# Kernel optimization log

Measured on AMD Instinct MI355X. Metric: run time of the kernel, lower is better.

The kernel has to match this reference:

```python
import jax, jax.numpy as jnp
import numpy as np

V, C, TCTX, H, L = 32000, 768, 1024, 12, 6
B, T = 2, 1024
D = C // H
EPS = 1e-5


def setup_inputs() -> dict:
    key = jax.random.key(0)
    ks = jax.random.split(key, 12)
    s = lambda k, shape: jax.random.normal(k, shape, jnp.float32) * 0.02
    return {
        "x_indices": jax.random.randint(ks[0], (B, T), 0, V, jnp.int32),
        "tok_emb": s(ks[1], (V, C)),
        "pos_emb": s(ks[2], (TCTX, C)),
        "ln1_g": jnp.ones((L, C)), "ln1_b": jnp.zeros((L, C)),
        "wq": s(ks[3], (L, C, C)), "wk": s(ks[4], (L, C, C)), "wv": s(ks[5], (L, C, C)),
        "wo": s(ks[6], (L, C, C)), "bo": jnp.zeros((L, C)),
        "ln2_g": jnp.ones((L, C)), "ln2_b": jnp.zeros((L, C)),
        "w1": s(ks[7], (L, C, 4 * C)), "b1": jnp.zeros((L, 4 * C)),
        "w2": s(ks[8], (L, 4 * C, C)), "b2": jnp.zeros((L, C)),
        "lnf_g": jnp.ones((C,)), "lnf_b": jnp.zeros((C,)),
        "wp": s(ks[9], (C, V)), "bp": jnp.zeros((V,)),
    }


def _ln(x, g, b):
    m = x.mean(-1, keepdims=True)
    v = ((x - m) ** 2).mean(-1, keepdims=True)
    return (x - m) * jax.lax.rsqrt(v + EPS) * g + b


def _forward(x_indices, tok_emb, pos_emb, ln1_g, ln1_b, wq, wk, wv, wo, bo,
             ln2_g, ln2_b, w1, b1, w2, b2, lnf_g, lnf_b, wp, bp):
    Bv, Tv = x_indices.shape
    x = tok_emb[x_indices] + pos_emb[:Tv]  # [B,T,C]
    mask = jnp.tril(jnp.ones((Tv, Tv), dtype=bool))  # causal

    def block(x, p):
        g1, be1, q_w, k_w, v_w, o_w, o_b, g2, be2, f1, fb1, f2, fb2 = p
        h = _ln(x, g1, be1)
        q = (h @ q_w).reshape(Bv, Tv, H, D)
        k = (h @ k_w).reshape(Bv, Tv, H, D)
        v = (h @ v_w).reshape(Bv, Tv, H, D)
        scores = jnp.einsum('bthd,bshd->bhts', q, k) / jnp.sqrt(jnp.float32(D))
        scores = jnp.where(mask, scores, -jnp.inf)
        a = jax.nn.softmax(scores, axis=-1)
        o = jnp.einsum('bhts,bshd->bthd', a, v).reshape(Bv, Tv, C)
        x = x + o @ o_w + o_b
        h2 = _ln(x, g2, be2)
        x = x + jax.nn.relu(h2 @ f1 + fb1) @ f2 + fb2
        return x, None

    layer_params = (ln1_g, ln1_b, wq, wk, wv, wo, bo, ln2_g, ln2_b, w1, b1, w2, b2)
    x, _ = jax.lax.scan(block, x, layer_params)
    x = _ln(x, lnf_g, lnf_b)
    return x @ wp + bp  # logits [B,T,V]


def reference(x_indices, tok_emb, pos_emb, ln1_g, ln1_b, wq, wk, wv, wo, bo,
              ln2_g, ln2_b, w1, b1, w2, b2, lnf_g, lnf_b, wp, bp):
    return _forward(x_indices, tok_emb, pos_emb, ln1_g, ln1_b, wq, wk, wv, wo, bo,
                    ln2_g, ln2_b, w1, b1, w2, b2, lnf_g, lnf_b, wp, bp)
```

## Files before the change

### kernel.cpp

```cpp
#include <hip/hip_runtime.h>
#include <stdint.h>

#define DEV __device__ __forceinline__

typedef unsigned short u16;
typedef __attribute__((ext_vector_type(8))) short short8;
typedef __attribute__((ext_vector_type(4))) float floatx4;

#define B_ 2
#define T_ 1024
#define C_ 768
#define H_ 12
#define L_ 6
#define V_ 32000
#define F_ 3072
#define M_ 2048
#define C3_ 2304

#define VMW(n) asm volatile("s_waitcnt vmcnt(" #n ")" ::: "memory")

DEV u16 f2bf(float f) {
  unsigned int u; __builtin_memcpy(&u, &f, 4);
  u += 0x7FFFu + ((u >> 16) & 1u);
  return (u16)(u >> 16);
}

DEV void gload16(const void* g, void* l) {
  __builtin_amdgcn_global_load_lds(
      (__attribute__((address_space(1))) void*)(uintptr_t)g,
      (__attribute__((address_space(3))) void*)(unsigned int)(uintptr_t)l,
      16, 0, 0);
}

DEV int xcd_swz(int flat, int nwg) {
  int q = nwg >> 3, r = nwg & 7;
  int xcd = flat & 7, sid = flat >> 3;
  return (xcd < r ? xcd * (q + 1) : r * (q + 1) + (xcd - r) * q) + sid;
}

__global__ __launch_bounds__(256) void transpose_f32_bf16(
    const float* __restrict__ src, u16* __restrict__ dst, int R, int Cc,
    size_t src_z, size_t dst_z) {
  __shared__ float tile[32][33];
  const float* s = src + (size_t)blockIdx.z * src_z;
  u16* d = dst + (size_t)blockIdx.z * dst_z;
  int c0 = blockIdx.x * 32, r0 = blockIdx.y * 32;
  int tx = threadIdx.x & 31, ty = threadIdx.x >> 5;
#pragma unroll
  for (int i = 0; i < 4; i++)
    tile[ty + 8 * i][tx] = s[(size_t)(r0 + ty + 8 * i) * Cc + (c0 + tx)];
  __syncthreads();
#pragma unroll
  for (int i = 0; i < 4; i++)
    d[(size_t)(c0 + ty + 8 * i) * R + (r0 + tx)] = f2bf(tile[tx][ty + 8 * i]);
}

__global__ __launch_bounds__(256) void embed_kernel(
    const int* __restrict__ idx, const float* __restrict__ tok,
    const float* __restrict__ pos, float* __restrict__ x) {
  int row = blockIdx.x;
  int t = row & (T_ - 1);
  int tk = idx[row];
  const float* tp = tok + (size_t)tk * C_;
  const float* pp = pos + (size_t)t * C_;
  float* xp = x + (size_t)row * C_;
  for (int c = threadIdx.x; c < C_; c += 256) xp[c] = tp[c] + pp[c];
}

__global__ __launch_bounds__(256) void ln_kernel(
    const float* __restrict__ x, const float* __restrict__ g,
    const float* __restrict__ b, u16* __restrict__ out) {
  int row = blockIdx.x;
  int tid = threadIdx.x;
  const float* xp = x + (size_t)row * C_;
  float v0 = xp[tid], v1 = xp[tid + 256], v2 = xp[tid + 512];
  float s = v0 + v1 + v2;
  float ss = v0 * v0 + v1 * v1 + v2 * v2;
#pragma unroll
  for (int o = 32; o > 0; o >>= 1) { s += __shfl_down(s, o); ss += __shfl_down(ss, o); }
  __shared__ float red[8];
  int wid = tid >> 6;
  if ((tid & 63) == 0) { red[wid] = s; red[4 + wid] = ss; }
  __syncthreads();
  float tot = red[0] + red[1] + red[2] + red[3];
  float tss = red[4] + red[5] + red[6] + red[7];
  float mean = tot * (1.f / C_);
  float var = tss * (1.f / C_) - mean * mean;
  float rstd = rsqrtf(var + 1e-5f);
  u16* op = out + (size_t)row * C_;
  op[tid]       = f2bf((v0 - mean) * rstd * g[tid]       + b[tid]);
  op[tid + 256] = f2bf((v1 - mean) * rstd * g[tid + 256] + b[tid + 256]);
  op[tid + 512] = f2bf((v2 - mean) * rstd * g[tid + 512] + b[tid + 512]);
}

template <int THREADS, int BM, int BN, int WM, int WN, int BIAS, int RELU, int OUTMODE, int SPLITK>
__global__ __launch_bounds__(THREADS) void gemm3(
    const u16* __restrict__ A, const u16* __restrict__ BT,
    const float* __restrict__ bias,
    u16* __restrict__ ob, float* __restrict__ fout, u16* __restrict__ vt,
    int N, int K) {
  constexpr int ALOADS = (BM * 64) / (THREADS * 16);
  constexpr int BLOADS = (BN * 64) / (THREADS * 16);
  constexpr int LDS_L = ALOADS + BLOADS;
  constexpr int MF = BM / (WM * 16);
  constexpr int NF = BN / (WN * 16);
  __shared__ __align__(16) u16 As[3][BM * 32];
  __shared__ __align__(16) u16 Bs[3][BN * 32];

  int tid = threadIdx.x;
  int lane = tid & 63, w = tid >> 6;
  int wm = w / WN, wn = w % WN;
  int rr = lane & 15, qg = lane >> 4;

  int gx = gridDim.x;
  int nwg = gx * gridDim.y;
  int flat = blockIdx.y * gx + blockIdx.x;
  int wg = xcd_swz(flat, nwg);
  int m0 = (wg % gx) * BM, n0 = (wg / gx) * BN;

  int kz = SPLITK > 1 ? blockIdx.z : 0;
  int Keff = SPLITK > 1 ? (K / SPLITK) : K;
  int kbase = kz * Keff;

  const u16* Aps[ALOADS];
  const u16* Bps[BLOADS];
#pragma unroll
  for (int i = 0; i < ALOADS; i++) {
    int idx = i * THREADS + tid;
    int row = idx >> 2;
    int chunk = (idx & 3) ^ ((row >> 1) & 3);
    Aps[i] = A + (size_t)(m0 + row) * K + chunk * 8 + kbase;
  }
#pragma unroll
  for (int i = 0; i < BLOADS; i++) {
    int idx = i * THREADS + tid;
    int row = idx >> 2;
    int chunk = (idx & 3) ^ ((row >> 1) & 3);
    Bps[i] = BT + (size_t)(n0 + row) * K + chunk * 8 + kbase;
  }

  auto stage = [&](int sl, int kk) {
#pragma unroll
    for (int i = 0; i < ALOADS; i++)
      gload16(Aps[i] + kk, (char*)As + (size_t)sl * BM * 64 + i * THREADS * 16 + w * 1024);
#pragma unroll
    for (int i = 0; i < BLOADS; i++)
      gload16(Bps[i] + kk, (char*)Bs + (size_t)sl * BN * 64 + i * THREADS * 16 + w * 1024);
  };

  floatx4 zero = {0.f, 0.f, 0.f, 0.f};
  floatx4 acc[MF][NF];
#pragma unroll
  for (int i = 0; i < MF; i++)
#pragma unroll
    for (int j = 0; j < NF; j++) acc[i][j] = zero;

  int NT = Keff >> 5;
  stage(0, 0);
  stage(1, 32);
  if constexpr (LDS_L == 3) VMW(3);
  else if constexpr (LDS_L == 4) VMW(4);
  else VMW(6);
  __builtin_amdgcn_s_barrier();
  __builtin_amdgcn_sched_barrier(0);

  int sqA = (qg ^ ((rr >> 1) & 3)) << 4;

  for (int t = 0; t < NT; ++t) {
    int sl = t % 3;
    if (t + 2 < NT) stage((t + 2) % 3, (t + 2) << 5);
    __builtin_amdgcn_sched_barrier(0);
    const char* Ab = (const char*)As + (size_t)sl * BM * 64;
    const char* Bb = (const char*)Bs + (size_t)sl * BN * 64;
    short8 af[MF], bf[NF];
#pragma unroll
    for (int i = 0; i < MF; i++)
      af[i] = *(const short8*)(Ab + ((wm * (BM / WM) + i * 16 + rr) << 6) + sqA);
#pragma unroll
    for (int j = 0; j < NF; j++)
      bf[j] = *(const short8*)(Bb + ((wn * (BN / WN) + j * 16 + rr) << 6) + sqA);
    __builtin_amdgcn_s_setprio(1);
#pragma unroll
    for (int i = 0; i < MF; i++)
#pragma unroll
      for (int j = 0; j < NF; j++)
        acc[i][j] = __builtin_amdgcn_mfma_f32_16x16x32_bf16(af[i], bf[j], acc[i][j], 0, 0, 0);
    __builtin_amdgcn_s_setprio(0);
    if (t < NT - 2) {
      if constexpr (LDS_L == 3) VMW(3);
      else if constexpr (LDS_L == 4) VMW(4);
      else VMW(6);
    } else if (t == NT - 2) VMW(0);
    if (t < NT - 1) { __builtin_amdgcn_s_barrier(); __builtin_amdgcn_sched_barrier(0); }
  }

  int cb = n0 + wn * (BN / WN);
  int rb = m0 + wm * (BM / WM);
  bool isv = (OUTMODE == 3) && (n0 >= 1536);
#pragma unroll
  for (int i = 0; i < MF; i++) {
#pragma unroll
    for (int j = 0; j < NF; j++) {
      int col = cb + j * 16 + rr;
      float bv = 0.f;
      if (BIAS && kz == 0) bv = bias[col];
      float vals[4];
#pragma unroll
      for (int r = 0; r < 4; r++) {
        float val = acc[i][j][r] + bv;
        if (RELU) val = fmaxf(val, 0.f);
        vals[r] = val;
      }
      int row0 = rb + i * 16 + qg * 4;
      if (isv) {
        int colv = col - 1536;
        int bb = row0 >> 10, t0 = row0 & (T_ - 1);
        uint2 pk;
        pk.x = (unsigned int)f2bf(vals[0]) | ((unsigned int)f2bf(vals[1]) << 16);
        pk.y = (unsigned int)f2bf(vals[2]) | ((unsigned int)f2bf(vals[3]) << 16);
        *(uint2*)&vt[((size_t)bb * C_ + colv) * T_ + t0] = pk;
      } else {
#pragma unroll
        for (int r = 0; r < 4; r++) {
          size_t o = (size_t)(row0 + r) * N + col;
          if (OUTMODE == 0 || OUTMODE == 3) ob[o] = f2bf(vals[r]);
          else if (OUTMODE == 1) {
            if (SPLITK > 1) atomicAdd(&fout[o], vals[r]);
            else fout[o] += vals[r];
          } else fout[o] = vals[r];
        }
      }
    }
  }
}

__global__ __launch_bounds__(512, 2) void gemm8(
    const u16* __restrict__ A, const u16* __restrict__ BT,
    const float* __restrict__ bias, float* __restrict__ fout, int N, int K) {
  __shared__ __align__(16) u16 As[2][2][256 * 32];
  __shared__ __align__(16) u16 Bs[2][2][256 * 32];
  int tid = threadIdx.x;
  int lane = tid & 63, w = tid >> 6;
  int wr = w >> 2, wc = w & 3;
  int rr = lane & 15, qg = lane >> 4;

  int gx = gridDim.x;
  int nwg = gx * gridDim.y;
  int flat = blockIdx.y * gx + blockIdx.x;
  int wg = xcd_swz(flat, nwg);
  int m0 = (wg % gx) * 256, n0 = (wg / gx) * 256;

  int r0 = tid >> 2;
  int c0 = (((tid & 3) ^ ((r0 >> 1) & 3)) << 3);
  int r1 = (512 + tid) >> 2;
  int c1 = (((tid & 3) ^ ((r1 >> 1) & 3)) << 3);
  const u16* Asrc0 = A + (size_t)(m0 + r0) * K + c0;
  const u16* Asrc1 = A + (size_t)(m0 + r1) * K + c1;
  const u16* Bsrc0 = BT + (size_t)(n0 + r0) * K + c0;
  const u16* Bsrc1 = BT + (size_t)(n0 + r1) * K + c1;

  auto stageA = [&](int s, int kh, int kt) {
    int koff = (kt << 6) + (kh << 5);
    gload16(Asrc0 + koff, (char*)&As[s][kh][0] + w * 1024);
    gload16(Asrc1 + koff, (char*)&As[s][kh][0] + 8192 + w * 1024);
  };
  auto stageB = [&](int s, int kh, int kt) {
    int koff = (kt << 6) + (kh << 5);
    gload16(Bsrc0 + koff, (char*)&Bs[s][kh][0] + w * 1024);
    gload16(Bsrc1 + koff, (char*)&Bs[s][kh][0] + 8192 + w * 1024);
  };

  floatx4 zero = {0.f, 0.f, 0.f, 0.f};
  floatx4 acc[8][4];
#pragma unroll
  for (int i = 0; i < 8; i++)
#pragma unroll
    for (int j = 0; j < 4; j++) acc[i][j] = zero;

  int NKT = K >> 6;
  stageA(0, 0, 0); stageB(0, 0, 0); stageA(0, 1, 0); stageB(0, 1, 0);
  VMW(0);
  __builtin_amdgcn_s_barrier();
  __builtin_amdgcn_sched_barrier(0);

  int sq = (qg ^ ((rr >> 1) & 3)) << 4;
  short8 bf[4];

  for (int kt = 0; kt < NKT; ++kt) {
    int d = kt & 1;
    bool more = (kt + 1) < NKT;
#pragma unroll
    for (int p = 0; p < 4; ++p) {
      const int kh = p >> 1, rh = p & 1;
      const char* Ab = (const char*)&As[d][kh][0];
      const char* Bb = (const char*)&Bs[d][kh][0];
      short8 af[4];
#pragma unroll
      for (int i = 0; i < 4; i++)
        af[i] = *(const short8*)(Ab + ((wr * 128 + rh * 64 + i * 16 + rr) << 6) + sq);
      if (rh == 0) {
#pragma unroll
        for (int j = 0; j < 4; j++)
          bf[j] = *(const short8*)(Bb + ((wc * 64 + j * 16 + rr) << 6) + sq);
      }
      if (more) {
        if (p == 0) stageA(d ^ 1, 0, kt + 1);
        else if (p == 1) stageB(d ^ 1, 0, kt + 1);
        else if (p == 2) stageA(d ^ 1, 1, kt + 1);
        else stageB(d ^ 1, 1, kt + 1);
      }
      __builtin_amdgcn_s_barrier();
      asm volatile("s_waitcnt lgkmcnt(0)" ::: "memory");
      __builtin_amdgcn_sched_barrier(0);
      __builtin_amdgcn_s_setprio(1);
#pragma unroll
      for (int i = 0; i < 4; i++)
#pragma unroll
        for (int j = 0; j < 4; j++)
          acc[rh * 4 + i][j] =
              __builtin_amdgcn_mfma_f32_16x16x32_bf16(af[i], bf[j], acc[rh * 4 + i][j], 0, 0, 0);
      __builtin_amdgcn_s_setprio(0);
      if (rh == 1) VMW(4);
      __builtin_amdgcn_s_barrier();
      __builtin_amdgcn_sched_barrier(0);
    }
  }

  int cb = n0 + wc * 64;
  int rb = m0 + wr * 128;
#pragma unroll
  for (int fi = 0; fi < 8; fi++) {
#pragma unroll
    for (int j = 0; j < 4; j++) {
      int col = cb + j * 16 + rr;
      float bv = bias[col];
      int row0 = rb + fi * 16 + qg * 4;
#pragma unroll
      for (int r = 0; r < 4; r++)
        fout[(size_t)(row0 + r) * N + col] = acc[fi][j][r] + bv;
    }
  }
}

__global__ __launch_bounds__(64) void attn_kernel(
    const u16* __restrict__ qkv, const u16* __restrict__ vt, u16* __restrict__ o) {
  __shared__ __align__(16) u16 P_s[16 * 48];
  int nwg = gridDim.x;
  int wg = xcd_swz(blockIdx.x, nwg);
  int qt = wg & 63;
  int h = (wg >> 6) % H_;
  int b = wg / (64 * H_);
  int q0 = qt << 4;
  int lane = threadIdx.x;
  int rr = lane & 15, qg = lane >> 4, kq = qg << 3;

  const u16* qb = qkv + (size_t)(b * T_ + q0 + rr) * C3_ + h * 64;
  short8 qf0 = *(const short8*)(qb + kq);
  short8 qf1 = *(const short8*)(qb + 32 + kq);

  float m_r = -1e30f, l_r = 0.f;
  floatx4 zero = {0.f, 0.f, 0.f, 0.f};
  floatx4 oacc[4];
#pragma unroll
  for (int d = 0; d < 4; d++) oacc[d] = zero;

  const u16* kbase = qkv + (size_t)(b * T_) * C3_ + 768 + h * 64;
  const u16* vbase = vt + (size_t)(b * C_ + h * 64) * T_;

  for (int kt0 = 0; kt0 <= q0 + 15; kt0 += 32) {
    floatx4 s[2];
#pragma unroll
    for (int c = 0; c < 2; c++) {
      const u16* kb = kbase + (size_t)(kt0 + c * 16 + rr) * C3_;
      short8 kf0 = *(const short8*)(kb + kq);
      short8 kf1 = *(const short8*)(kb + 32 + kq);
      floatx4 z = zero;
      z = __builtin_amdgcn_mfma_f32_16x16x32_bf16(kf0, qf0, z, 0, 0, 0);
      z = __builtin_amdgcn_mfma_f32_16x16x32_bf16(kf1, qf1, z, 0, 0, 0);
      s[c] = z;
    }
    int qpos = q0 + rr;
    float p[2][4];
    float mx = -1e30f;
#pragma unroll
    for (int c = 0; c < 2; c++)
#pragma unroll
      for (int r = 0; r < 4; r++) {
        int kpos = kt0 + c * 16 + qg * 4 + r;
        float val = s[c][r] * 0.125f;
        val = (kpos <= qpos) ? val : -1e30f;
        p[c][r] = val;
        mx = fmaxf(mx, val);
      }
    mx = fmaxf(mx, __shfl_xor(mx, 16));
    mx = fmaxf(mx, __shfl_xor(mx, 32));
    float mn = fmaxf(m_r, mx);
    float escL = exp2f((m_r - mn) * 1.44269504f);
    m_r = mn;
    float ps = 0.f;
#pragma unroll
    for (int c = 0; c < 2; c++)
#pragma unroll
      for (int r = 0; r < 4; r++) {
        float pv = exp2f((p[c][r] - mn) * 1.44269504f);
        p[c][r] = pv;
        ps += pv;
      }
    ps += __shfl_xor(ps, 16);
    ps += __shfl_xor(ps, 32);
    l_r = l_r * escL + ps;
#pragma unroll
    for (int c = 0; c < 2; c++) {
      unsigned int u0 = (unsigned int)f2bf(p[c][0]) | ((unsigned int)f2bf(p[c][1]) << 16);
      unsigned int u1 = (unsigned int)f2bf(p[c][2]) | ((unsigned int)f2bf(p[c][3]) << 16);
      uint2 pk; pk.x = u0; pk.y = u1;
      *(uint2*)&P_s[rr * 48 + c * 16 + qg * 4] = pk;
    }
    float er[4];
#pragma unroll
    for (int r = 0; r < 4; r++) er[r] = __shfl(escL, qg * 4 + r);
#pragma unroll
    for (int d = 0; d < 4; d++)
#pragma unroll
      for (int r = 0; r < 4; r++) oacc[d][r] *= er[r];
    short8 pa = *(const short8*)&P_s[rr * 48 + kq];
#pragma unroll
    for (int d = 0; d < 4; d++) {
      short8 vf = *(const short8*)(vbase + (size_t)(d * 16 + rr) * T_ + kt0 + kq);
      oacc[d] = __builtin_amdgcn_mfma_f32_16x16x32_bf16(pa, vf, oacc[d], 0, 0, 0);
    }
  }
  float lb[4];
#pragma unroll
  for (int r = 0; r < 4; r++) lb[r] = __shfl(l_r, qg * 4 + r);
  u16* obp = o + (size_t)(b * T_ + q0) * C_ + h * 64;
#pragma unroll
  for (int d = 0; d < 4; d++)
#pragma unroll
    for (int r = 0; r < 4; r++) {
      int row = qg * 4 + r;
      obp[(size_t)row * C_ + d * 16 + rr] = f2bf(oacc[d][r] / lb[r]);
    }
}

extern "C" void kernel_launch(void* const* d_in, const int* in_sizes, int n_in,
                              void* d_out, int out_size, void* d_ws, size_t ws_size,
                              hipStream_t stream) {
  (void)in_sizes; (void)n_in; (void)out_size; (void)ws_size;
  const int*   xidx = (const int*)d_in[0];
  const float* tok  = (const float*)d_in[1];
  const float* pos  = (const float*)d_in[2];
  const float* ln1g = (const float*)d_in[3];
  const float* ln1b = (const float*)d_in[4];
  const float* wq   = (const float*)d_in[5];
  const float* wk   = (const float*)d_in[6];
  const float* wv   = (const float*)d_in[7];
  const float* wo   = (const float*)d_in[8];
  const float* bo   = (const float*)d_in[9];
  const float* ln2g = (const float*)d_in[10];
  const float* ln2b = (const float*)d_in[11];
  const float* w1   = (const float*)d_in[12];
  const float* b1   = (const float*)d_in[13];
  const float* w2   = (const float*)d_in[14];
  const float* b2   = (const float*)d_in[15];
  const float* lnfg = (const float*)d_in[16];
  const float* lnfb = (const float*)d_in[17];
  const float* wp   = (const float*)d_in[18];
  const float* bp   = (const float*)d_in[19];

  char* ws = (char*)d_ws;
  size_t off = 0;
  auto alloc = [&](size_t bytes) { char* p = ws + off; off += (bytes + 255) & ~(size_t)255; return p; };
  u16* wqkvT = (u16*)alloc((size_t)L_ * 3 * C_ * C_ * 2);
  u16* woT = (u16*)alloc((size_t)L_ * C_ * C_ * 2);
  u16* w1T = (u16*)alloc((size_t)L_ * C_ * F_ * 2);
  u16* w2T = (u16*)alloc((size_t)L_ * C_ * F_ * 2);
  u16* wpT = (u16*)alloc((size_t)C_ * V_ * 2);
  float* x = (float*)alloc((size_t)M_ * C_ * 4);
  u16* hb   = (u16*)alloc((size_t)M_ * C_ * 2);
  u16* qkvb = (u16*)alloc((size_t)M_ * C3_ * 2);
  u16* vtb  = (u16*)alloc((size_t)M_ * C_ * 2);
  u16* aob  = (u16*)alloc((size_t)M_ * C_ * 2);
  u16* mb   = (u16*)alloc((size_t)M_ * F_ * 2);

  dim3 blk(256);
  size_t CC = (size_t)C_ * C_, CF = (size_t)C_ * F_;
  transpose_f32_bf16<<<dim3(C_ / 32, C_ / 32, L_), blk, 0, stream>>>(wq, wqkvT,          C_, C_, CC, 3 * CC);
  transpose_f32_bf16<<<dim3(C_ / 32, C_ / 32, L_), blk, 0, stream>>>(wk, wqkvT + CC,     C_, C_, CC, 3 * CC);
  transpose_f32_bf16<<<dim3(C_ / 32, C_ / 32, L_), blk, 0, stream>>>(wv, wqkvT + 2 * CC, C_, C_, CC, 3 * CC);
  transpose_f32_bf16<<<dim3(C_ / 32, C_ / 32, L_), blk, 0, stream>>>(wo, woT, C_, C_, CC, CC);
  transpose_f32_bf16<<<dim3(F_ / 32, C_ / 32, L_), blk, 0, stream>>>(w1, w1T, C_, F_, CF, CF);
  transpose_f32_bf16<<<dim3(C_ / 32, F_ / 32, L_), blk, 0, stream>>>(w2, w2T, F_, C_, CF, CF);
  transpose_f32_bf16<<<dim3(V_ / 32, C_ / 32, 1), blk, 0, stream>>>(wp, wpT, C_, V_, 0, 0);
  embed_kernel<<<M_, blk, 0, stream>>>(xidx, tok, pos, x);

  for (int l = 0; l < L_; ++l) {
    size_t wOff = (size_t)l * 3 * CC;
    size_t oOff = (size_t)l * CC;
    size_t fOff = (size_t)l * CF;
    ln_kernel<<<M_, blk, 0, stream>>>(x, ln1g + l * C_, ln1b + l * C_, hb);
    gemm3<256, 128, 128, 2, 2, 0, 0, 3, 1><<<dim3(M_ / 128, C3_ / 128), 256, 0, stream>>>(
        hb, wqkvT + wOff, nullptr, qkvb, nullptr, vtb, C3_, C_);
    attn_kernel<<<B_ * H_ * (T_ / 16), dim3(64), 0, stream>>>(qkvb, vtb, aob);
    gemm3<256, 128, 128, 2, 2, 1, 0, 1, 2><<<dim3(M_ / 128, C_ / 128, 2), 256, 0, stream>>>(
        aob, woT + oOff, bo + l * C_, nullptr, x, nullptr, C_, C_);
    ln_kernel<<<M_, blk, 0, stream>>>(x, ln2g + l * C_, ln2b + l * C_, hb);
    gemm3<256, 128, 128, 2, 2, 1, 1, 0, 1><<<dim3(M_ / 128, F_ / 128), 256, 0, stream>>>(
        hb, w1T + fOff, b1 + l * F_, mb, nullptr, nullptr, F_, C_);
    gemm3<256, 128, 128, 2, 2, 1, 0, 1, 2><<<dim3(M_ / 128, C_ / 128, 2), 256, 0, stream>>>(
        mb, w2T + fOff, b2 + l * C_, nullptr, x, nullptr, C_, F_);
  }
  ln_kernel<<<M_, blk, 0, stream>>>(x, lnfg, lnfb, hb);
  gemm8<<<dim3(M_ / 256, V_ / 256), 512, 0, stream>>>(
      hb, wpT, bp, (float*)d_out, V_, C_);
}
```

Baseline: 1.074 ms.

## Software-pipeline LDS fragment reads in vocab GEMM and shrink layer GEMM tiles

The vocab projection GEMM now double-buffers its A/B register fragments. It issues the LDS reads for the next sub-step before running the MFMAs for the current one, and moves the global prefetch stages so the LDS read latency hides behind compute with fewer barriers. Its launch bound no longer forces two blocks per CU, which lets the compiler use more registers. The per-layer GEMMs switch from 128x128 to 64x64 tiles to launch more workgroups across the CUs. The smaller tiles add load traffic per FLOP and may raise split-K atomic counts.

Result: slower. 1.123 ms (+4.5%).

```diff
diff --git a/kernel.cpp b/kernel.cpp
--- a/kernel.cpp
+++ b/kernel.cpp
@@ -18,6 +18,9 @@
 #define C3_ 2304
 
 #define VMW(n) asm volatile("s_waitcnt vmcnt(" #n ")" ::: "memory")
+#define LGKM0 asm volatile("s_waitcnt lgkmcnt(0)" ::: "memory")
+#define SBAR __builtin_amdgcn_s_barrier()
+#define SCHED0 __builtin_amdgcn_sched_barrier(0)
 
 DEV u16 f2bf(float f) {
   unsigned int u; __builtin_memcpy(&u, &f, 4);
@@ -158,18 +161,19 @@
   int NT = Keff >> 5;
   stage(0, 0);
   stage(1, 32);
-  if constexpr (LDS_L == 3) VMW(3);
+  if constexpr (LDS_L == 2) VMW(2);
+  else if constexpr (LDS_L == 3) VMW(3);
   else if constexpr (LDS_L == 4) VMW(4);
   else VMW(6);
-  __builtin_amdgcn_s_barrier();
-  __builtin_amdgcn_sched_barrier(0);
+  SBAR;
+  SCHED0;
 
   int sqA = (qg ^ ((rr >> 1) & 3)) << 4;
 
   for (int t = 0; t < NT; ++t) {
     int sl = t % 3;
     if (t + 2 < NT) stage((t + 2) % 3, (t + 2) << 5);
-    __builtin_amdgcn_sched_barrier(0);
+    SCHED0;
     const char* Ab = (const char*)As + (size_t)sl * BM * 64;
     const char* Bb = (const char*)Bs + (size_t)sl * BN * 64;
     short8 af[MF], bf[NF];
@@ -187,11 +191,12 @@
         acc[i][j] = __builtin_amdgcn_mfma_f32_16x16x32_bf16(af[i], bf[j], acc[i][j], 0, 0, 0);
     __builtin_amdgcn_s_setprio(0);
     if (t < NT - 2) {
-      if constexpr (LDS_L == 3) VMW(3);
+      if constexpr (LDS_L == 2) VMW(2);
+      else if constexpr (LDS_L == 3) VMW(3);
       else if constexpr (LDS_L == 4) VMW(4);
       else VMW(6);
     } else if (t == NT - 2) VMW(0);
-    if (t < NT - 1) { __builtin_amdgcn_s_barrier(); __builtin_amdgcn_sched_barrier(0); }
+    if (t < NT - 1) { SBAR; SCHED0; }
   }
 
   int cb = n0 + wn * (BN / WN);
@@ -234,7 +239,7 @@
   }
 }
 
-__global__ __launch_bounds__(512, 2) void gemm8(
+__global__ __launch_bounds__(512) void gemm8(
     const u16* __restrict__ A, const u16* __restrict__ BT,
     const float* __restrict__ bias, float* __restrict__ fout, int N, int K) {
   __shared__ __align__(16) u16 As[2][2][256 * 32];
@@ -270,6 +275,22 @@
     gload16(Bsrc1 + koff, (char*)&Bs[s][kh][0] + 8192 + w * 1024);
   };
 
+  int sq = (qg ^ ((rr >> 1) & 3)) << 4;
+  short8 afb[2][4], bfb[2][4];
+
+  auto readAf = [&](short8* dst, int d2, int kh, int rh) {
+    const char* Ab = (const char*)&As[d2][kh][0];
+#pragma unroll
+    for (int i = 0; i < 4; i++)
+      dst[i] = *(const short8*)(Ab + ((wr * 128 + rh * 64 + i * 16 + rr) << 6) + sq);
+  };
+  auto readBf = [&](short8* dst, int d2, int kh) {
+    const char* Bb = (const char*)&Bs[d2][kh][0];
+#pragma unroll
+    for (int j = 0; j < 4; j++)
+      dst[j] = *(const short8*)(Bb + ((wc * 64 + j * 16 + rr) << 6) + sq);
+  };
+
   floatx4 zero = {0.f, 0.f, 0.f, 0.f};
   floatx4 acc[8][4];
 #pragma unroll
@@ -279,50 +300,45 @@
 
   int NKT = K >> 6;
   stageA(0, 0, 0); stageB(0, 0, 0); stageA(0, 1, 0); stageB(0, 1, 0);
-  VMW(0);
-  __builtin_amdgcn_s_barrier();
-  __builtin_amdgcn_sched_barrier(0);
-
-  int sq = (qg ^ ((rr >> 1) & 3)) << 4;
-  short8 bf[4];
+  VMW(4);
+  SBAR;
+  readAf(afb[0], 0, 0, 0);
+  readBf(bfb[0], 0, 0);
+  LGKM0;
+  SCHED0;
 
   for (int kt = 0; kt < NKT; ++kt) {
     int d = kt & 1;
     bool more = (kt + 1) < NKT;
 #pragma unroll
     for (int p = 0; p < 4; ++p) {
-      const int kh = p >> 1, rh = p & 1;
-      const char* Ab = (const char*)&As[d][kh][0];
-      const char* Bb = (const char*)&Bs[d][kh][0];
-      short8 af[4];
+      if (more) {
+        if (p == 0) { stageA(d ^ 1, 0, kt + 1); stageB(d ^ 1, 0, kt + 1); }
+        else if (p == 1) stageA(d ^ 1, 1, kt + 1);
+        else if (p == 2) stageB(d ^ 1, 1, kt + 1);
+      }
+      if (p < 3) {
+        readAf(afb[(p + 1) & 1], d, (p + 1) >> 1, (p + 1) & 1);
+        if (p == 1) readBf(bfb[1], d, 1);
+      } else if (more) {
+        readAf(afb[0], d ^ 1, 0, 0);
+        readBf(bfb[0], d ^ 1, 0);
+      }
+      SCHED0;
+      __builtin_amdgcn_s_setprio(1);
 #pragma unroll
       for (int i = 0; i < 4; i++)
-        af[i] = *(const short8*)(Ab + ((wr * 128 + rh * 64 + i * 16 + rr) << 6) + sq);
-      if (rh == 0) {
 #pragma unroll
         for (int j = 0; j < 4; j++)
-          bf[j] = *(const short8*)(Bb + ((wc * 64 + j * 16 + rr) << 6) + sq);
-      }
-      if (more) {
-        if (p == 0) stageA(d ^ 1, 0, kt + 1);
-        else if (p == 1) stageB(d ^ 1, 0, kt + 1);
-        else if (p == 2) stageA(d ^ 1, 1, kt + 1);
-        else stageB(d ^ 1, 1, kt + 1);
-      }
-      __builtin_amdgcn_s_barrier();
-      asm volatile("s_waitcnt lgkmcnt(0)" ::: "memory");
-      __builtin_amdgcn_sched_barrier(0);
-      __builtin_amdgcn_s_setprio(1);
-#pragma unroll
-      for (int i = 0; i < 4; i++)
-#pragma unroll
-        for (int j = 0; j < 4; j++)
-          acc[rh * 4 + i][j] =
-              __builtin_amdgcn_mfma_f32_16x16x32_bf16(af[i], bf[j], acc[rh * 4 + i][j], 0, 0, 0);
+          acc[(p & 1) * 4 + i][j] = __builtin_amdgcn_mfma_f32_16x16x32_bf16(
+              afb[p & 1][i], bfb[p >> 1][j], acc[(p & 1) * 4 + i][j], 0, 0, 0);
       __builtin_amdgcn_s_setprio(0);
-      if (rh == 1) VMW(4);
-      __builtin_amdgcn_s_barrier();
-      __builtin_amdgcn_sched_barrier(0);
+      LGKM0;
+      SCHED0;
+      if (p == 0) { if (more) VMW(4); else VMW(0); }
+      else if (p == 2) { if (more) VMW(4); }
+      SBAR;
+      SCHED0;
     }
   }
 
@@ -499,15 +515,15 @@
     size_t oOff = (size_t)l * CC;
     size_t fOff = (size_t)l * CF;
     ln_kernel<<<M_, blk, 0, stream>>>(x, ln1g + l * C_, ln1b + l * C_, hb);
-    gemm3<256, 128, 128, 2, 2, 0, 0, 3, 1><<<dim3(M_ / 128, C3_ / 128), 256, 0, stream>>>(
+    gemm3<256, 64, 64, 2, 2, 0, 0, 3, 1><<<dim3(M_ / 64, C3_ / 64), 256, 0, stream>>>(
         hb, wqkvT + wOff, nullptr, qkvb, nullptr, vtb, C3_, C_);
     attn_kernel<<<B_ * H_ * (T_ / 16), dim3(64), 0, stream>>>(qkvb, vtb, aob);
-    gemm3<256, 128, 128, 2, 2, 1, 0, 1, 2><<<dim3(M_ / 128, C_ / 128, 2), 256, 0, stream>>>(
+    gemm3<256, 64, 64, 2, 2, 1, 0, 1, 2><<<dim3(M_ / 64, C_ / 64, 2), 256, 0, stream>>>(
         aob, woT + oOff, bo + l * C_, nullptr, x, nullptr, C_, C_);
     ln_kernel<<<M_, blk, 0, stream>>>(x, ln2g + l * C_, ln2b + l * C_, hb);
-    gemm3<256, 128, 128, 2, 2, 1, 1, 0, 1><<<dim3(M_ / 128, F_ / 128), 256, 0, stream>>>(
+    gemm3<256, 64, 64, 2, 2, 1, 1, 0, 1><<<dim3(M_ / 64, F_ / 64), 256, 0, stream>>>(
         hb, w1T + fOff, b1 + l * F_, mb, nullptr, nullptr, F_, C_);
-    gemm3<256, 128, 128, 2, 2, 1, 0, 1, 2><<<dim3(M_ / 128, C_ / 128, 2), 256, 0, stream>>>(
+    gemm3<256, 64, 64, 2, 2, 1, 0, 1, 2><<<dim3(M_ / 64, C_ / 64, 2), 256, 0, stream>>>(
         mb, w2T + fOff, b2 + l * C_, nullptr, x, nullptr, C_, F_);
   }
   ln_kernel<<<M_, blk, 0, stream>>>(x, lnfg, lnfb, hb);
```
